# Performance work log

Hardware: AMD Instinct MI355X
Metric: run time of the kernel (lower is better)

The kernel has to match this reference:

```python
import jax, jax.numpy as jnp
import numpy as np

MAX_SEQ_LENGTH = 32
LN_EPS = 1e-5


def setup_inputs() -> dict:
    key = jax.random.key(0)
    ks = jax.random.split(key, 6)
    N, T, D, H, O = 256, 1024, 128, 256, 128
    G = 4 * H
    # torch kaiming_normal_ on a 2D (in, 4H) tensor: fan_in = size(1) = 4H, std = sqrt(2/fan_in)
    std_k = float(np.sqrt(2.0 / G))
    X = jax.random.normal(ks[0], (N, T, D), dtype=jnp.float32)
    Wx = jax.random.normal(ks[1], (D, G), dtype=jnp.float32) * std_k
    Wh = jax.random.normal(ks[2], (H, G), dtype=jnp.float32) * std_k
    b = jnp.zeros((G,), dtype=jnp.float32)
    W1 = jax.random.normal(ks[3], (H, H), dtype=jnp.float32) * float(np.sqrt(1.0 / H))
    b1 = jnp.zeros((H,), dtype=jnp.float32)
    ln_gamma = jnp.ones((H,), dtype=jnp.float32)
    ln_beta = jnp.zeros((H,), dtype=jnp.float32)
    W2 = jax.random.normal(ks[4], (H, O), dtype=jnp.float32) * float(np.sqrt(1.0 / H))
    b2 = jnp.zeros((O,), dtype=jnp.float32)
    return {"X": X, "Wx": Wx, "Wh": Wh, "b": b, "W1": W1, "b1": b1,
            "ln_gamma": ln_gamma, "ln_beta": ln_beta, "W2": W2, "b2": b2}


def _fc(h, W1, b1, ln_gamma, ln_beta, W2, b2):
    z = h @ W1 + b1
    mu = jnp.mean(z, axis=-1, keepdims=True)
    var = jnp.var(z, axis=-1, keepdims=True)
    z = (z - mu) * jax.lax.rsqrt(var + LN_EPS) * ln_gamma + ln_beta
    z = jax.nn.relu(z)
    return z @ W2 + b2


def reference(X, Wx, Wh, b, W1, b1, ln_gamma, ln_beta, W2, b2):
    N, T, D = X.shape
    H = Wh.shape[0]
    h0 = jnp.zeros((N, H), dtype=X.dtype)
    c0 = jnp.zeros((N, H), dtype=X.dtype)

    # --- encoder: standard LSTM cell (sigmoid/tanh gates) ---
    def enc_step(carry, x_t):
        h, c = carry
        fm = x_t @ Wx + h @ Wh + b  # (N, 4H)
        i = jax.nn.sigmoid(fm[:, 0:H])
        f = jax.nn.sigmoid(fm[:, H:2 * H])
        o = jax.nn.sigmoid(fm[:, 2 * H:3 * H])
        g = jnp.tanh(fm[:, 3 * H:4 * H])
        c = c * f + i * g
        h = o * jnp.tanh(c)
        return (h, c), None

    (h, c), _ = jax.lax.scan(enc_step, (h0, c0), jnp.swapaxes(X, 0, 1))

    # --- decoder: NOTE original code uses RAW gate slices (no sigmoid/tanh),
    # and start_token is zeros so the start_token @ Wx term is exactly 0. ---
    def dec_step(carry, _):
        h, c = carry
        fm = h @ Wh + b  # zeros @ Wx contributes 0
        i = fm[:, 0:H]
        f = fm[:, H:2 * H]
        o = fm[:, 2 * H:3 * H]
        g = fm[:, 3 * H:4 * H]
        c = c * f + i * g
        h = o * jnp.tanh(c)
        y = _fc(h, W1, b1, ln_gamma, ln_beta, W2, b2)
        return (h, c), y

    _, ys = jax.lax.scan(dec_step, (h, c), None, length=MAX_SEQ_LENGTH)
    return jnp.swapaxes(ys, 0, 1)  # (N, max_seq_length, output_dim)
```

## Files before the change

kernel.cpp:

```cpp
#include <hip/hip_runtime.h>
#include <cmath>

typedef _Float16 f16;
typedef _Float16 f16x4v __attribute__((ext_vector_type(4)));
typedef _Float16 f16x8v __attribute__((ext_vector_type(8)));
typedef float f32x4v __attribute__((ext_vector_type(4)));

#define NTHR 256
#define WPG  16

__device__ __forceinline__ float sigmoidf_(float x) { return 1.0f / (1.0f + expf(-x)); }

__device__ __forceinline__ void store_sc(float* p, float v) {
  asm volatile("global_store_dword %0, %1, off sc0 sc1" :: "v"(p), "v"(v) : "memory");
}

__device__ __forceinline__ void ld4_sc(const float* p,
                                       float4& a, float4& b, float4& c, float4& d) {
  asm volatile(
      "global_load_dwordx4 %0, %4, off sc0 sc1\n\t"
      "global_load_dwordx4 %1, %5, off sc0 sc1\n\t"
      "global_load_dwordx4 %2, %6, off sc0 sc1\n\t"
      "global_load_dwordx4 %3, %7, off sc0 sc1\n\t"
      "s_waitcnt vmcnt(0)"
      : "=&v"(a), "=&v"(b), "=&v"(c), "=&v"(d)
      : "v"(p), "v"(p + 1024), "v"(p + 2048), "v"(p + 3072)
      : "memory");
}

__device__ __forceinline__ void arrive_bar(unsigned* cg) {
  asm volatile("s_waitcnt vmcnt(0)" ::: "memory");
  __syncthreads();
  if (threadIdx.x == 0)
    (void)__hip_atomic_fetch_add(cg, 1u, __ATOMIC_RELAXED, __HIP_MEMORY_SCOPE_AGENT);
}

__device__ __forceinline__ void wait_bar(unsigned* cg, unsigned target) {
  if (threadIdx.x == 0) {
    unsigned guard = 0;
    while (__hip_atomic_load(cg, __ATOMIC_RELAXED, __HIP_MEMORY_SCOPE_AGENT) < target) {
      __builtin_amdgcn_s_sleep(1);
      if (++guard > (1u << 22)) break;
    }
  }
  __syncthreads();
}

__device__ __forceinline__ void conv4_wr(float4 v, f16* ph, f16* pl) {
  f16x4v h, l;
  h[0] = (f16)v.x; h[1] = (f16)v.y; h[2] = (f16)v.z; h[3] = (f16)v.w;
  l[0] = (f16)(v.x - (float)h[0]); l[1] = (f16)(v.y - (float)h[1]);
  l[2] = (f16)(v.z - (float)h[2]); l[3] = (f16)(v.w - (float)h[3]);
  *(f16x4v*)ph = h; *(f16x4v*)pl = l;
}

__device__ __forceinline__ void conv8_wr(float4 a, float4 b, f16* ph, f16* pl) {
  f16x8v h, l;
  h[0]=(f16)a.x; h[1]=(f16)a.y; h[2]=(f16)a.z; h[3]=(f16)a.w;
  h[4]=(f16)b.x; h[5]=(f16)b.y; h[6]=(f16)b.z; h[7]=(f16)b.w;
  l[0]=(f16)(a.x-(float)h[0]); l[1]=(f16)(a.y-(float)h[1]);
  l[2]=(f16)(a.z-(float)h[2]); l[3]=(f16)(a.w-(float)h[3]);
  l[4]=(f16)(b.x-(float)h[4]); l[5]=(f16)(b.y-(float)h[5]);
  l[6]=(f16)(b.z-(float)h[6]); l[7]=(f16)(b.w-(float)h[7]);
  *(f16x8v*)ph = h; *(f16x8v*)pl = l;
}

__global__ __launch_bounds__(NTHR, 1) void lstm_k(
    const float* __restrict__ X,  const float* __restrict__ Wx,
    const float* __restrict__ Wh, const float* __restrict__ Bg,
    const float* __restrict__ W1, const float* __restrict__ B1,
    const float* __restrict__ LNG, const float* __restrict__ LNB,
    const float* __restrict__ W2, const float* __restrict__ B2,
    float* __restrict__ Y, unsigned* __restrict__ CNT,
    float* __restrict__ hbuf, float* __restrict__ zbuf)
{
  __shared__ f16   A_hi[16][392];
  __shared__ f16   A_lo[16][392];
  __shared__ float fm_lds[16][65];
  __shared__ float hst[16][260];
  __shared__ float w1_lds[16][268];
  __shared__ float w2_lds[8][268];
  __shared__ float lng_lds[256], lnb_lds[256];
  __shared__ float ln_mu[16], ln_rs[16];

  const int tid = threadIdx.x;
  const int wg  = blockIdx.x;
  const int g   = wg & 15;
  const int jm  = wg >> 4;
  const int n0  = g * 16;
  const int k0  = jm * 16;
  unsigned* cg  = CNT + g * 32;

  const int l     = tid & 63;
  const int w     = __builtin_amdgcn_readfirstlane(tid >> 6);
  const int krow0 = (l >> 4) * 8;
  const int arow  = l & 15;

  f16x8v Bh[12], Bl[12];
  {
    const int bcol = w * 256 + k0 + (l & 15);
    #pragma unroll
    for (int kt = 0; kt < 12; ++kt) {
      #pragma unroll
      for (int j = 0; j < 8; ++j) {
        int k = kt * 32 + krow0 + j;
        float v = (kt < 4) ? Wx[k * 1024 + bcol] : Wh[(k - 128) * 1024 + bcol];
        f16 hi = (f16)v;
        Bh[kt][j] = hi;
        Bl[kt][j] = (f16)(v - (float)hi);
      }
    }
  }

  for (int idx = tid; idx < 256 * 16; idx += NTHR) {
    int k = idx >> 4, cc = idx & 15;
    w1_lds[cc][k] = W1[k * 256 + k0 + cc];
  }
  for (int idx = tid; idx < 256 * 8; idx += NTHR) {
    int k = idx >> 3, cc = idx & 7;
    w2_lds[cc][k] = W2[k * 128 + jm * 8 + cc];
  }
  lng_lds[tid] = LNG[tid];
  lnb_lds[tid] = LNB[tid];

  const int gr = tid >> 4, gk = tid & 15;
  const float bias0 = Bg[      k0 + gk];
  const float bias1 = Bg[256 + k0 + gk];
  const float bias2 = Bg[512 + k0 + gk];
  const float bias3 = Bg[768 + k0 + gk];
  const float b1reg = B1[k0 + gk];
  const float b2reg = (tid < 128) ? B2[jm * 8 + (tid & 7)] : 0.0f;
  float c_reg = 0.0f;

  {
    const float* xp = X + (size_t)(n0 + (tid >> 4)) * 131072 + (size_t)(tid & 15) * 8;
    float4 xa = *(const float4*)xp;
    float4 xb = *(const float4*)(xp + 4);
    conv8_wr(xa, xb, &A_hi[tid >> 4][(tid & 15) * 8], &A_lo[tid >> 4][(tid & 15) * 8]);
    f16x8v z8 = {0,0,0,0,0,0,0,0};
    *(f16x8v*)&A_hi[tid >> 4][128 + (tid & 15) * 16] = z8;
    *(f16x8v*)&A_hi[tid >> 4][136 + (tid & 15) * 16] = z8;
    *(f16x8v*)&A_lo[tid >> 4][128 + (tid & 15) * 16] = z8;
    *(f16x8v*)&A_lo[tid >> 4][136 + (tid & 15) * 16] = z8;
  }
  __syncthreads();

  auto stage_h_A = [&](const float* hs) {
    float4 v0, v1, v2, v3;
    ld4_sc(hs, v0, v1, v2, v3);
    conv4_wr(v0, &A_hi[w     ][128 + 4 * l], &A_lo[w     ][128 + 4 * l]);
    conv4_wr(v1, &A_hi[w + 4 ][128 + 4 * l], &A_lo[w + 4 ][128 + 4 * l]);
    conv4_wr(v2, &A_hi[w + 8 ][128 + 4 * l], &A_lo[w + 8 ][128 + 4 * l]);
    conv4_wr(v3, &A_hi[w + 12][128 + 4 * l], &A_lo[w + 12][128 + 4 * l]);
  };

  for (int t = 0; t < 1024; ++t) {
    float4 xa, xb;
    if (t < 1023) {
      const float* xp = X + (size_t)(n0 + (tid >> 4)) * 131072
                          + (size_t)(t + 1) * 128 + (size_t)(tid & 15) * 8;
      xa = *(const float4*)xp;
      xb = *(const float4*)(xp + 4);
    }

    f32x4v ac0 = {0,0,0,0}, ac1 = {0,0,0,0}, ac2 = {0,0,0,0};
    {
      f16x8v xh[4], xl[4];
      const f16* pah = &A_hi[arow][krow0];
      const f16* pal = &A_lo[arow][krow0];
      #pragma unroll
      for (int kt = 0; kt < 4; ++kt) {
        xh[kt] = *(const f16x8v*)(pah + kt * 32);
        xl[kt] = *(const f16x8v*)(pal + kt * 32);
      }
      #pragma unroll
      for (int kt = 0; kt < 4; ++kt) {
        ac0 = __builtin_amdgcn_mfma_f32_16x16x32_f16(xh[kt], Bh[kt], ac0, 0, 0, 0);
        ac1 = __builtin_amdgcn_mfma_f32_16x16x32_f16(xh[kt], Bl[kt], ac1, 0, 0, 0);
        ac2 = __builtin_amdgcn_mfma_f32_16x16x32_f16(xl[kt], Bh[kt], ac2, 0, 0, 0);
      }
    }

    if (t > 0) {
      wait_bar(cg, (unsigned)(WPG * t));
      stage_h_A(hbuf + (size_t)((t - 1) & 1) * 65536 + (size_t)n0 * 256 + (size_t)tid * 4);
      __syncthreads();
    }

    {
      f16x8v hh[8], hl[8];
      const f16* pah = &A_hi[arow][128 + krow0];
      const f16* pal = &A_lo[arow][128 + krow0];
      #pragma unroll
      for (int kt = 0; kt < 8; ++kt) {
        hh[kt] = *(const f16x8v*)(pah + kt * 32);
        hl[kt] = *(const f16x8v*)(pal + kt * 32);
      }
      #pragma unroll
      for (int kt = 0; kt < 8; ++kt) {
        ac0 = __builtin_amdgcn_mfma_f32_16x16x32_f16(hh[kt], Bh[kt + 4], ac0, 0, 0, 0);
        ac1 = __builtin_amdgcn_mfma_f32_16x16x32_f16(hh[kt], Bl[kt + 4], ac1, 0, 0, 0);
        ac2 = __builtin_amdgcn_mfma_f32_16x16x32_f16(hl[kt], Bh[kt + 4], ac2, 0, 0, 0);
      }
    }
    #pragma unroll
    for (int q = 0; q < 4; ++q)
      fm_lds[(l >> 4) * 4 + q][w * 16 + (l & 15)] = ac0[q] + ac1[q] + ac2[q];
    __syncthreads();

    {
      float fi = fm_lds[gr][     gk] + bias0;
      float ff = fm_lds[gr][16 + gk] + bias1;
      float fo = fm_lds[gr][32 + gk] + bias2;
      float fg = fm_lds[gr][48 + gk] + bias3;
      float si = sigmoidf_(fi), sf = sigmoidf_(ff), so = sigmoidf_(fo);
      float tg = tanhf(fg);
      c_reg = c_reg * sf + si * tg;
      float hv = so * tanhf(c_reg);
      store_sc(hbuf + (size_t)(t & 1) * 65536 + (size_t)(n0 + gr) * 256 + k0 + gk, hv);
    }

    if (t < 1023)
      conv8_wr(xa, xb, &A_hi[tid >> 4][(tid & 15) * 8], &A_lo[tid >> 4][(tid & 15) * 8]);

    arrive_bar(cg);
  }

  wait_bar(cg, (unsigned)(WPG * 1024));
  stage_h_A(hbuf + (size_t)65536  + (size_t)n0 * 256 + (size_t)tid * 4);
  __syncthreads();
  unsigned arr = 1024;

  for (int s = 0; s < 32; ++s) {
    const int t = 1024 + s;

    f16x8v ah[8], al[8];
    {
      const f16* pah = &A_hi[arow][128 + krow0];
      const f16* pal = &A_lo[arow][128 + krow0];
      #pragma unroll
      for (int kt = 0; kt < 8; ++kt) {
        ah[kt] = *(const f16x8v*)(pah + kt * 32);
        al[kt] = *(const f16x8v*)(pal + kt * 32);
      }
    }
    f32x4v ac0 = {0,0,0,0}, ac1 = {0,0,0,0}, ac2 = {0,0,0,0};
    #pragma unroll
    for (int kt = 0; kt < 8; ++kt) {
      ac0 = __builtin_amdgcn_mfma_f32_16x16x32_f16(ah[kt], Bh[kt + 4], ac0, 0, 0, 0);
      ac1 = __builtin_amdgcn_mfma_f32_16x16x32_f16(ah[kt], Bl[kt + 4], ac1, 0, 0, 0);
      ac2 = __builtin_amdgcn_mfma_f32_16x16x32_f16(al[kt], Bh[kt + 4], ac2, 0, 0, 0);
    }
    #pragma unroll
    for (int q = 0; q < 4; ++q)
      fm_lds[(l >> 4) * 4 + q][w * 16 + (l & 15)] = ac0[q] + ac1[q] + ac2[q];
    __syncthreads();

    {
      float fi = fm_lds[gr][     gk] + bias0;
      float ff = fm_lds[gr][16 + gk] + bias1;
      float fo = fm_lds[gr][32 + gk] + bias2;
      float fg = fm_lds[gr][48 + gk] + bias3;
      c_reg = c_reg * ff + fi * fg;
      float hv = fo * tanhf(c_reg);
      store_sc(hbuf + (size_t)(t & 1) * 65536 + (size_t)(n0 + gr) * 256 + k0 + gk, hv);
    }
    arrive_bar(cg); ++arr;
    wait_bar(cg, WPG * arr);

    {
      const float* hs = hbuf + (size_t)(t & 1) * 65536 + (size_t)n0 * 256 + (size_t)tid * 4;
      float4 v0, v1, v2, v3;
      ld4_sc(hs, v0, v1, v2, v3);
      *(float4*)&hst[w     ][4 * l] = v0;
      *(float4*)&hst[w + 4 ][4 * l] = v1;
      *(float4*)&hst[w + 8 ][4 * l] = v2;
      *(float4*)&hst[w + 12][4 * l] = v3;
      conv4_wr(v0, &A_hi[w     ][128 + 4 * l], &A_lo[w     ][128 + 4 * l]);
      conv4_wr(v1, &A_hi[w + 4 ][128 + 4 * l], &A_lo[w + 4 ][128 + 4 * l]);
      conv4_wr(v2, &A_hi[w + 8 ][128 + 4 * l], &A_lo[w + 8 ][128 + 4 * l]);
      conv4_wr(v3, &A_hi[w + 12][128 + 4 * l], &A_lo[w + 12][128 + 4 * l]);
    }
    __syncthreads();

    {
      float za = b1reg;
      const float* hr = &hst[gr][0];
      const float* wr = &w1_lds[gk][0];
      #pragma unroll 4
      for (int kc = 0; kc < 64; ++kc) {
        float4 h4 = *(const float4*)(hr + kc * 4);
        float4 w4 = *(const float4*)(wr + kc * 4);
        za = fmaf(h4.x, w4.x, fmaf(h4.y, w4.y, fmaf(h4.z, w4.z, fmaf(h4.w, w4.w, za))));
      }
      store_sc(zbuf + (size_t)(n0 + gr) * 256 + k0 + gk, za);
    }
    arrive_bar(cg); ++arr;
    wait_bar(cg, WPG * arr);

    {
      const float* zs = zbuf + (size_t)n0 * 256 + (size_t)tid * 4;
      float4 v0, v1, v2, v3;
      ld4_sc(zs, v0, v1, v2, v3);
      *(float4*)&hst[w     ][4 * l] = v0;
      *(float4*)&hst[w + 4 ][4 * l] = v1;
      *(float4*)&hst[w + 8 ][4 * l] = v2;
      *(float4*)&hst[w + 12][4 * l] = v3;
    }
    __syncthreads();

    {
      const float* zr = &hst[gr][0];
      float s1 = 0.f, s2 = 0.f;
      #pragma unroll
      for (int u = 0; u < 16; ++u) { float v = zr[gk * 16 + u]; s1 += v; s2 += v * v; }
      #pragma unroll
      for (int d = 1; d < 16; d <<= 1) { s1 += __shfl_xor(s1, d); s2 += __shfl_xor(s2, d); }
      float mu = s1 * (1.0f / 256.0f);
      float var = s2 * (1.0f / 256.0f) - mu * mu;
      float rstd = rsqrtf(var + 1e-5f);
      if (gk == 0) { ln_mu[gr] = mu; ln_rs[gr] = rstd; }
    }
    __syncthreads();

    #pragma unroll
    for (int rep = 0; rep < 4; ++rep) {
      int f = tid + 256 * rep, r = f >> 6, kq = f & 63;
      float mu = ln_mu[r], rs = ln_rs[r];
      float4 v = *(float4*)&hst[r][kq * 4];
      int cb = kq * 4;
      v.x = fmaxf(fmaf((v.x - mu) * rs, lng_lds[cb    ], lnb_lds[cb    ]), 0.f);
      v.y = fmaxf(fmaf((v.y - mu) * rs, lng_lds[cb + 1], lnb_lds[cb + 1]), 0.f);
      v.z = fmaxf(fmaf((v.z - mu) * rs, lng_lds[cb + 2], lnb_lds[cb + 2]), 0.f);
      v.w = fmaxf(fmaf((v.w - mu) * rs, lng_lds[cb + 3], lnb_lds[cb + 3]), 0.f);
      *(float4*)&hst[r][kq * 4] = v;
    }
    __syncthreads();

    if (tid < 128) {
      int r = tid >> 3, yc = tid & 7;
      float ya = b2reg;
      const float* zr = &hst[r][0];
      const float* wr = &w2_lds[yc][0];
      #pragma unroll 4
      for (int kc = 0; kc < 64; ++kc) {
        float4 z4 = *(const float4*)(zr + kc * 4);
        float4 w4 = *(const float4*)(wr + kc * 4);
        ya = fmaf(z4.x, w4.x, fmaf(z4.y, w4.y, fmaf(z4.z, w4.z, fmaf(z4.w, w4.w, ya))));
      }
      Y[(size_t)(n0 + r) * 4096 + (size_t)s * 128 + jm * 8 + yc] = ya;
    }
  }
}

extern "C" void kernel_launch(void* const* d_in, const int* in_sizes, int n_in,
                              void* d_out, int out_size, void* d_ws, size_t ws_size,
                              hipStream_t stream) {
  const float* X   = (const float*)d_in[0];
  const float* Wx  = (const float*)d_in[1];
  const float* Wh  = (const float*)d_in[2];
  const float* b   = (const float*)d_in[3];
  const float* W1  = (const float*)d_in[4];
  const float* b1  = (const float*)d_in[5];
  const float* lng = (const float*)d_in[6];
  const float* lnb = (const float*)d_in[7];
  const float* W2  = (const float*)d_in[8];
  const float* b2  = (const float*)d_in[9];
  float* Y = (float*)d_out;

  unsigned* cnt = (unsigned*)d_ws;
  float* hbuf = (float*)((char*)d_ws + 2048);
  float* zbuf = hbuf + 2 * 256 * 256;
  (void)in_sizes; (void)n_in; (void)out_size; (void)ws_size;

  hipMemsetAsync(d_ws, 0, 2048, stream);
  hipLaunchKernelGGL(lstm_k, dim3(256), dim3(NTHR), 0, stream,
                     X, Wx, Wh, b, W1, b1, lng, lnb, W2, b2, Y, cnt, hbuf, zbuf);
}
```

Before: 2.991 ms.

## Remap gate columns per wave, pack h as hi/lo f16 pairs, use fast transcendentals

Each wave now owns all four gates for its own set of hidden columns, so the gate nonlinearity reads a per-wave LDS scratch and the block-wide __syncthreads between the MFMA and the cell update is gone. The hidden state is exchanged through global memory already split into packed f16 hi/lo halves, so readers unpack it with integer ops instead of converting fp32. Sigmoid and tanh switch to exp2/rcp intrinsics with input clamping. These aim to cut per-step latency on the serial recurrence, at some risk to accuracy from the approximate math.

```diff
diff --git a/kernel.cpp b/kernel.cpp
--- a/kernel.cpp
+++ b/kernel.cpp
@@ -2,21 +2,55 @@
 #include <cmath>
 
 typedef _Float16 f16;
-typedef _Float16 f16x4v __attribute__((ext_vector_type(4)));
 typedef _Float16 f16x8v __attribute__((ext_vector_type(8)));
 typedef float f32x4v __attribute__((ext_vector_type(4)));
 
 #define NTHR 256
 #define WPG  16
 
-__device__ __forceinline__ float sigmoidf_(float x) { return 1.0f / (1.0f + expf(-x)); }
-
-__device__ __forceinline__ void store_sc(float* p, float v) {
+__device__ __forceinline__ float fexp2_(float x) {
+#if __has_builtin(__builtin_amdgcn_exp2f)
+  return __builtin_amdgcn_exp2f(x);
+#else
+  return exp2f(x);
+#endif
+}
+__device__ __forceinline__ float frcp_(float x) {
+#if __has_builtin(__builtin_amdgcn_rcpf)
+  return __builtin_amdgcn_rcpf(x);
+#else
+  return 1.0f / x;
+#endif
+}
+__device__ __forceinline__ float fsigmoid(float x) {
+  float xc = fminf(fmaxf(x, -60.f), 60.f);
+  return frcp_(1.f + fexp2_(xc * -1.44269504f));
+}
+__device__ __forceinline__ float ftanh_(float x) {
+  float xc = fminf(fmaxf(x, -15.f), 15.f);
+  float e = fexp2_(xc * 2.88539008f);
+  return (e - 1.f) * frcp_(e + 1.f);
+}
+
+__device__ __forceinline__ void st_sc_u(unsigned* p, unsigned v) {
   asm volatile("global_store_dword %0, %1, off sc0 sc1" :: "v"(p), "v"(v) : "memory");
 }
-
-__device__ __forceinline__ void ld4_sc(const float* p,
-                                       float4& a, float4& b, float4& c, float4& d) {
+__device__ __forceinline__ void st_sc_f(float* p, float v) {
+  asm volatile("global_store_dword %0, %1, off sc0 sc1" :: "v"(p), "v"(v) : "memory");
+}
+
+__device__ __forceinline__ void ld64u_sc(const unsigned* p, uint4& a, uint4& b,
+                                         uint4& c, uint4& d) {
+  asm volatile(
+      "global_load_dwordx4 %0, %4, off sc0 sc1\n\t"
+      "global_load_dwordx4 %1, %4, off offset:16 sc0 sc1\n\t"
+      "global_load_dwordx4 %2, %4, off offset:32 sc0 sc1\n\t"
+      "global_load_dwordx4 %3, %4, off offset:48 sc0 sc1\n\t"
+      "s_waitcnt vmcnt(0)"
+      : "=&v"(a), "=&v"(b), "=&v"(c), "=&v"(d) : "v"(p) : "memory");
+}
+__device__ __forceinline__ void ld4f_sc(const float* p, float4& a, float4& b,
+                                        float4& c, float4& d) {
   asm volatile(
       "global_load_dwordx4 %0, %4, off sc0 sc1\n\t"
       "global_load_dwordx4 %1, %5, off sc0 sc1\n\t"
@@ -24,8 +58,7 @@
       "global_load_dwordx4 %3, %7, off sc0 sc1\n\t"
       "s_waitcnt vmcnt(0)"
       : "=&v"(a), "=&v"(b), "=&v"(c), "=&v"(d)
-      : "v"(p), "v"(p + 1024), "v"(p + 2048), "v"(p + 3072)
-      : "memory");
+      : "v"(p), "v"(p + 1024), "v"(p + 2048), "v"(p + 3072) : "memory");
 }
 
 __device__ __forceinline__ void arrive_bar(unsigned* cg) {
@@ -34,7 +67,6 @@
   if (threadIdx.x == 0)
     (void)__hip_atomic_fetch_add(cg, 1u, __ATOMIC_RELAXED, __HIP_MEMORY_SCOPE_AGENT);
 }
-
 __device__ __forceinline__ void wait_bar(unsigned* cg, unsigned target) {
   if (threadIdx.x == 0) {
     unsigned guard = 0;
@@ -46,14 +78,27 @@
   __syncthreads();
 }
 
-__device__ __forceinline__ void conv4_wr(float4 v, f16* ph, f16* pl) {
-  f16x4v h, l;
-  h[0] = (f16)v.x; h[1] = (f16)v.y; h[2] = (f16)v.z; h[3] = (f16)v.w;
-  l[0] = (f16)(v.x - (float)h[0]); l[1] = (f16)(v.y - (float)h[1]);
-  l[2] = (f16)(v.z - (float)h[2]); l[3] = (f16)(v.w - (float)h[3]);
-  *(f16x4v*)ph = h; *(f16x4v*)pl = l;
-}
-
+__device__ __forceinline__ unsigned packhl(float v) {
+  f16 h = (f16)v;
+  f16 lo = (f16)(v - (float)h);
+  unsigned short hb, lb;
+  __builtin_memcpy(&hb, &h, 2); __builtin_memcpy(&lb, &lo, 2);
+  return (unsigned)hb | ((unsigned)lb << 16);
+}
+__device__ __forceinline__ float unpackf(unsigned u) {
+  unsigned short hb = (unsigned short)(u & 0xffffu), lb = (unsigned short)(u >> 16);
+  f16 h, l;
+  __builtin_memcpy(&h, &hb, 2); __builtin_memcpy(&l, &lb, 2);
+  return (float)h + (float)l;
+}
+__device__ __forceinline__ void unpack_wr(uint4 c, f16* ph, f16* pl) {
+  unsigned h01 = (c.x & 0xffffu) | (c.y << 16);
+  unsigned h23 = (c.z & 0xffffu) | (c.w << 16);
+  unsigned l01 = (c.x >> 16) | (c.y & 0xffff0000u);
+  unsigned l23 = (c.z >> 16) | (c.w & 0xffff0000u);
+  uint2 hh = {h01, h23}, ll = {l01, l23};
+  *(uint2*)ph = hh; *(uint2*)pl = ll;
+}
 __device__ __forceinline__ void conv8_wr(float4 a, float4 b, f16* ph, f16* pl) {
   f16x8v h, l;
   h[0]=(f16)a.x; h[1]=(f16)a.y; h[2]=(f16)a.z; h[3]=(f16)a.w;
@@ -72,11 +117,11 @@
     const float* __restrict__ LNG, const float* __restrict__ LNB,
     const float* __restrict__ W2, const float* __restrict__ B2,
     float* __restrict__ Y, unsigned* __restrict__ CNT,
-    float* __restrict__ hbuf, float* __restrict__ zbuf)
+    unsigned* __restrict__ HBp, float* __restrict__ ZB)
 {
   __shared__ f16   A_hi[16][392];
   __shared__ f16   A_lo[16][392];
-  __shared__ float fm_lds[16][65];
+  __shared__ float fm_w[4][16][20];
   __shared__ float hst[16][260];
   __shared__ float w1_lds[16][268];
   __shared__ float w2_lds[8][268];
@@ -92,13 +137,17 @@
   unsigned* cg  = CNT + g * 32;
 
   const int l     = tid & 63;
-  const int w     = __builtin_amdgcn_readfirstlane(tid >> 6);
+  const int wv    = __builtin_amdgcn_readfirstlane(tid >> 6);
+  const int arow  = l & 15;
   const int krow0 = (l >> 4) * 8;
-  const int arow  = l & 15;
+
+  const int qq = (l >> 2) & 3;
+  const int hc = l & 3;
+  const int ch = k0 + 4 * wv + hc;
 
   f16x8v Bh[12], Bl[12];
   {
-    const int bcol = w * 256 + k0 + (l & 15);
+    const int bcol = qq * 256 + ch;
     #pragma unroll
     for (int kt = 0; kt < 12; ++kt) {
       #pragma unroll
@@ -123,35 +172,37 @@
   lng_lds[tid] = LNG[tid];
   lnb_lds[tid] = LNB[tid];
 
+  const float biasI = Bg[        ch];
+  const float biasF = Bg[256   + ch];
+  const float biasO = Bg[512   + ch];
+  const float biasG = Bg[768   + ch];
+  const int   myrow = (l >> 4) * 4 + qq;
+  float c_reg = 0.0f;
+
   const int gr = tid >> 4, gk = tid & 15;
-  const float bias0 = Bg[      k0 + gk];
-  const float bias1 = Bg[256 + k0 + gk];
-  const float bias2 = Bg[512 + k0 + gk];
-  const float bias3 = Bg[768 + k0 + gk];
   const float b1reg = B1[k0 + gk];
   const float b2reg = (tid < 128) ? B2[jm * 8 + (tid & 7)] : 0.0f;
-  float c_reg = 0.0f;
 
   {
     const float* xp = X + (size_t)(n0 + (tid >> 4)) * 131072 + (size_t)(tid & 15) * 8;
-    float4 xa = *(const float4*)xp;
-    float4 xb = *(const float4*)(xp + 4);
-    conv8_wr(xa, xb, &A_hi[tid >> 4][(tid & 15) * 8], &A_lo[tid >> 4][(tid & 15) * 8]);
+    conv8_wr(*(const float4*)xp, *(const float4*)(xp + 4),
+             &A_hi[tid >> 4][(tid & 15) * 8], &A_lo[tid >> 4][(tid & 15) * 8]);
     f16x8v z8 = {0,0,0,0,0,0,0,0};
-    *(f16x8v*)&A_hi[tid >> 4][128 + (tid & 15) * 16] = z8;
-    *(f16x8v*)&A_hi[tid >> 4][136 + (tid & 15) * 16] = z8;
-    *(f16x8v*)&A_lo[tid >> 4][128 + (tid & 15) * 16] = z8;
-    *(f16x8v*)&A_lo[tid >> 4][136 + (tid & 15) * 16] = z8;
+    *(f16x8v*)&A_hi[tid >> 4][128 + (tid & 15) * 16]     = z8;
+    *(f16x8v*)&A_hi[tid >> 4][128 + (tid & 15) * 16 + 8] = z8;
+    *(f16x8v*)&A_lo[tid >> 4][128 + (tid & 15) * 16]     = z8;
+    *(f16x8v*)&A_lo[tid >> 4][128 + (tid & 15) * 16 + 8] = z8;
   }
   __syncthreads();
 
-  auto stage_h_A = [&](const float* hs) {
-    float4 v0, v1, v2, v3;
-    ld4_sc(hs, v0, v1, v2, v3);
-    conv4_wr(v0, &A_hi[w     ][128 + 4 * l], &A_lo[w     ][128 + 4 * l]);
-    conv4_wr(v1, &A_hi[w + 4 ][128 + 4 * l], &A_lo[w + 4 ][128 + 4 * l]);
-    conv4_wr(v2, &A_hi[w + 8 ][128 + 4 * l], &A_lo[w + 8 ][128 + 4 * l]);
-    conv4_wr(v3, &A_hi[w + 12][128 + 4 * l], &A_lo[w + 12][128 + 4 * l]);
+  auto stage_hA = [&](const unsigned* hb) {
+    const int row = tid >> 4, cb = (tid & 15) * 16;
+    uint4 c0, c1, c2, c3;
+    ld64u_sc(hb + (size_t)row * 256 + cb, c0, c1, c2, c3);
+    unpack_wr(c0, &A_hi[row][128 + cb],      &A_lo[row][128 + cb]);
+    unpack_wr(c1, &A_hi[row][128 + cb + 4],  &A_lo[row][128 + cb + 4]);
+    unpack_wr(c2, &A_hi[row][128 + cb + 8],  &A_lo[row][128 + cb + 8]);
+    unpack_wr(c3, &A_hi[row][128 + cb + 12], &A_lo[row][128 + cb + 12]);
   };
 
   for (int t = 0; t < 1024; ++t) {
@@ -183,7 +234,7 @@
 
     if (t > 0) {
       wait_bar(cg, (unsigned)(WPG * t));
-      stage_h_A(hbuf + (size_t)((t - 1) & 1) * 65536 + (size_t)n0 * 256 + (size_t)tid * 4);
+      stage_hA(HBp + (size_t)((t - 1) & 1) * 65536 + (size_t)n0 * 256);
       __syncthreads();
     }
 
@@ -203,83 +254,86 @@
         ac2 = __builtin_amdgcn_mfma_f32_16x16x32_f16(hl[kt], Bh[kt + 4], ac2, 0, 0, 0);
       }
     }
-    #pragma unroll
-    for (int q = 0; q < 4; ++q)
-      fm_lds[(l >> 4) * 4 + q][w * 16 + (l & 15)] = ac0[q] + ac1[q] + ac2[q];
-    __syncthreads();
-
-    {
-      float fi = fm_lds[gr][     gk] + bias0;
-      float ff = fm_lds[gr][16 + gk] + bias1;
-      float fo = fm_lds[gr][32 + gk] + bias2;
-      float fg = fm_lds[gr][48 + gk] + bias3;
-      float si = sigmoidf_(fi), sf = sigmoidf_(ff), so = sigmoidf_(fo);
-      float tg = tanhf(fg);
+
+    {
+      f32x4v ac = ac0 + ac1 + ac2;
+      *(f32x4v*)&fm_w[wv][l & 15][(l >> 4) * 4] = ac;
+      float fi = fm_w[wv][     hc][myrow] + biasI;
+      float ff = fm_w[wv][ 4 + hc][myrow] + biasF;
+      float fo = fm_w[wv][ 8 + hc][myrow] + biasO;
+      float fg = fm_w[wv][12 + hc][myrow] + biasG;
+      float si = fsigmoid(fi), sf = fsigmoid(ff), so = fsigmoid(fo);
+      float tg = ftanh_(fg);
       c_reg = c_reg * sf + si * tg;
-      float hv = so * tanhf(c_reg);
-      store_sc(hbuf + (size_t)(t & 1) * 65536 + (size_t)(n0 + gr) * 256 + k0 + gk, hv);
-    }
-
+      float hv = so * ftanh_(c_reg);
+      st_sc_u(HBp + (size_t)(t & 1) * 65536 + (size_t)(n0 + myrow) * 256 + ch,
+              packhl(hv));
+    }
+
+    if (t == 0) __syncthreads();
     if (t < 1023)
       conv8_wr(xa, xb, &A_hi[tid >> 4][(tid & 15) * 8], &A_lo[tid >> 4][(tid & 15) * 8]);
-
     arrive_bar(cg);
   }
 
   wait_bar(cg, (unsigned)(WPG * 1024));
-  stage_h_A(hbuf + (size_t)65536  + (size_t)n0 * 256 + (size_t)tid * 4);
+  stage_hA(HBp + (size_t)65536 + (size_t)n0 * 256);
   __syncthreads();
   unsigned arr = 1024;
 
   for (int s = 0; s < 32; ++s) {
     const int t = 1024 + s;
 
-    f16x8v ah[8], al[8];
-    {
+    f32x4v ac0 = {0,0,0,0}, ac1 = {0,0,0,0}, ac2 = {0,0,0,0};
+    {
+      f16x8v hh[8], hl[8];
       const f16* pah = &A_hi[arow][128 + krow0];
       const f16* pal = &A_lo[arow][128 + krow0];
       #pragma unroll
       for (int kt = 0; kt < 8; ++kt) {
-        ah[kt] = *(const f16x8v*)(pah + kt * 32);
-        al[kt] = *(const f16x8v*)(pal + kt * 32);
-      }
-    }
-    f32x4v ac0 = {0,0,0,0}, ac1 = {0,0,0,0}, ac2 = {0,0,0,0};
-    #pragma unroll
-    for (int kt = 0; kt < 8; ++kt) {
-      ac0 = __builtin_amdgcn_mfma_f32_16x16x32_f16(ah[kt], Bh[kt + 4], ac0, 0, 0, 0);
-      ac1 = __builtin_amdgcn_mfma_f32_16x16x32_f16(ah[kt], Bl[kt + 4], ac1, 0, 0, 0);
-      ac2 = __builtin_amdgcn_mfma_f32_16x16x32_f16(al[kt], Bh[kt + 4], ac2, 0, 0, 0);
-    }
-    #pragma unroll
-    for (int q = 0; q < 4; ++q)
-      fm_lds[(l >> 4) * 4 + q][w * 16 + (l & 15)] = ac0[q] + ac1[q] + ac2[q];
-    __syncthreads();
-
-    {
-      float fi = fm_lds[gr][     gk] + bias0;
-      float ff = fm_lds[gr][16 + gk] + bias1;
-      float fo = fm_lds[gr][32 + gk] + bias2;
-      float fg = fm_lds[gr][48 + gk] + bias3;
+        hh[kt] = *(const f16x8v*)(pah + kt * 32);
+        hl[kt] = *(const f16x8v*)(pal + kt * 32);
+      }
+      #pragma unroll
+      for (int kt = 0; kt < 8; ++kt) {
+        ac0 = __builtin_amdgcn_mfma_f32_16x16x32_f16(hh[kt], Bh[kt + 4], ac0, 0, 0, 0);
+        ac1 = __builtin_amdgcn_mfma_f32_16x16x32_f16(hh[kt], Bl[kt + 4], ac1, 0, 0, 0);
+        ac2 = __builtin_amdgcn_mfma_f32_16x16x32_f16(hl[kt], Bh[kt + 4], ac2, 0, 0, 0);
+      }
+    }
+    {
+      f32x4v ac = ac0 + ac1 + ac2;
+      *(f32x4v*)&fm_w[wv][l & 15][(l >> 4) * 4] = ac;
+      float fi = fm_w[wv][     hc][myrow] + biasI;
+      float ff = fm_w[wv][ 4 + hc][myrow] + biasF;
+      float fo = fm_w[wv][ 8 + hc][myrow] + biasO;
+      float fg = fm_w[wv][12 + hc][myrow] + biasG;
       c_reg = c_reg * ff + fi * fg;
-      float hv = fo * tanhf(c_reg);
-      store_sc(hbuf + (size_t)(t & 1) * 65536 + (size_t)(n0 + gr) * 256 + k0 + gk, hv);
+      float hv = fo * ftanh_(c_reg);
+      st_sc_u(HBp + (size_t)(t & 1) * 65536 + (size_t)(n0 + myrow) * 256 + ch,
+              packhl(hv));
     }
     arrive_bar(cg); ++arr;
     wait_bar(cg, WPG * arr);
 
     {
-      const float* hs = hbuf + (size_t)(t & 1) * 65536 + (size_t)n0 * 256 + (size_t)tid * 4;
-      float4 v0, v1, v2, v3;
-      ld4_sc(hs, v0, v1, v2, v3);
-      *(float4*)&hst[w     ][4 * l] = v0;
-      *(float4*)&hst[w + 4 ][4 * l] = v1;
-      *(float4*)&hst[w + 8 ][4 * l] = v2;
-      *(float4*)&hst[w + 12][4 * l] = v3;
-      conv4_wr(v0, &A_hi[w     ][128 + 4 * l], &A_lo[w     ][128 + 4 * l]);
-      conv4_wr(v1, &A_hi[w + 4 ][128 + 4 * l], &A_lo[w + 4 ][128 + 4 * l]);
-      conv4_wr(v2, &A_hi[w + 8 ][128 + 4 * l], &A_lo[w + 8 ][128 + 4 * l]);
-      conv4_wr(v3, &A_hi[w + 12][128 + 4 * l], &A_lo[w + 12][128 + 4 * l]);
+      const int row = tid >> 4, cb = (tid & 15) * 16;
+      const unsigned* hb = HBp + (size_t)(t & 1) * 65536 + (size_t)n0 * 256
+                               + (size_t)row * 256 + cb;
+      uint4 c0, c1, c2, c3;
+      ld64u_sc(hb, c0, c1, c2, c3);
+      unpack_wr(c0, &A_hi[row][128 + cb],      &A_lo[row][128 + cb]);
+      unpack_wr(c1, &A_hi[row][128 + cb + 4],  &A_lo[row][128 + cb + 4]);
+      unpack_wr(c2, &A_hi[row][128 + cb + 8],  &A_lo[row][128 + cb + 8]);
+      unpack_wr(c3, &A_hi[row][128 + cb + 12], &A_lo[row][128 + cb + 12]);
+      float4 f0 = {unpackf(c0.x), unpackf(c0.y), unpackf(c0.z), unpackf(c0.w)};
+      float4 f1 = {unpackf(c1.x), unpackf(c1.y), unpackf(c1.z), unpackf(c1.w)};
+      float4 f2 = {unpackf(c2.x), unpackf(c2.y), unpackf(c2.z), unpackf(c2.w)};
+      float4 f3 = {unpackf(c3.x), unpackf(c3.y), unpackf(c3.z), unpackf(c3.w)};
+      *(float4*)&hst[row][cb]      = f0;
+      *(float4*)&hst[row][cb + 4]  = f1;
+      *(float4*)&hst[row][cb + 8]  = f2;
+      *(float4*)&hst[row][cb + 12] = f3;
     }
     __syncthreads();
 
@@ -293,19 +347,20 @@
         float4 w4 = *(const float4*)(wr + kc * 4);
         za = fmaf(h4.x, w4.x, fmaf(h4.y, w4.y, fmaf(h4.z, w4.z, fmaf(h4.w, w4.w, za))));
       }
-      store_sc(zbuf + (size_t)(n0 + gr) * 256 + k0 + gk, za);
+      st_sc_f(ZB + (size_t)(n0 + gr) * 256 + k0 + gk, za);
     }
     arrive_bar(cg); ++arr;
     wait_bar(cg, WPG * arr);
 
     {
-      const float* zs = zbuf + (size_t)n0 * 256 + (size_t)tid * 4;
+      const float* zs = ZB + (size_t)n0 * 256 + (size_t)tid * 4;
       float4 v0, v1, v2, v3;
-      ld4_sc(zs, v0, v1, v2, v3);
-      *(float4*)&hst[w     ][4 * l] = v0;
-      *(float4*)&hst[w + 4 ][4 * l] = v1;
-      *(float4*)&hst[w + 8 ][4 * l] = v2;
-      *(float4*)&hst[w + 12][4 * l] = v3;
+      ld4f_sc(zs, v0, v1, v2, v3);
+      const int w0 = tid >> 6, cl = (tid & 63) * 4;
+      *(float4*)&hst[w0     ][cl] = v0;
+      *(float4*)&hst[w0 + 4 ][cl] = v1;
+      *(float4*)&hst[w0 + 8 ][cl] = v2;
+      *(float4*)&hst[w0 + 12][cl] = v3;
     }
     __syncthreads();
 
@@ -350,6 +405,7 @@
       }
       Y[(size_t)(n0 + r) * 4096 + (size_t)s * 128 + jm * 8 + yc] = ya;
     }
+    __syncthreads();
   }
 }
 
@@ -368,12 +424,12 @@
   const float* b2  = (const float*)d_in[9];
   float* Y = (float*)d_out;
 
-  unsigned* cnt = (unsigned*)d_ws;
-  float* hbuf = (float*)((char*)d_ws + 2048);
-  float* zbuf = hbuf + 2 * 256 * 256;
+  unsigned* CNTp = (unsigned*)d_ws;
+  unsigned* HBp  = (unsigned*)((char*)d_ws + 4096);
+  float*    ZB   = (float*)((char*)d_ws + 4096 + 524288);
   (void)in_sizes; (void)n_in; (void)out_size; (void)ws_size;
 
   hipMemsetAsync(d_ws, 0, 2048, stream);
   hipLaunchKernelGGL(lstm_k, dim3(256), dim3(NTHR), 0, stream,
-                     X, Wx, Wh, b, W1, b1, lng, lnb, W2, b2, Y, cnt, hbuf, zbuf);
-}
+                     X, Wx, Wh, b, W1, b1, lng, lnb, W2, b2, Y, CNTp, HBp, ZB);
+}
```

New measurement: 2.885 ms. 3.5% less time.
